# Kernel tuning notes

Hardware: AMD Instinct MI355X
Metric: run time of the kernel (lower is better)

## Reference

```python
import jax, jax.numpy as jnp
import numpy as np

B, T, DIM = 1, 1024, 1024
H = 8
QLR, KVLR = 768, 512
DNOPE, DROPE, DV = 128, 64, 128
DK = DNOPE + DROPE  # 192
EPS = 1e-5


def _rms(x, w):
    return x * jax.lax.rsqrt(jnp.mean(x * x, axis=-1, keepdims=True) + EPS) * w


def _l2norm(x):
    return x * jax.lax.rsqrt(jnp.sum(x * x, axis=-1, keepdims=True) + 1e-6)


def setup_inputs() -> dict:
    key = jax.random.key(0)
    ks = jax.random.split(key, 12)
    std = 0.02
    rnd = lambda k, shape: (jax.random.normal(k, shape, dtype=jnp.float32) * std)
    return {
        'x': jax.random.normal(ks[0], (B, T, DIM), dtype=jnp.float32),
        'cos': jax.random.normal(ks[1], (T, DROPE), dtype=jnp.float32),
        'sin': jax.random.normal(ks[2], (T, DROPE), dtype=jnp.float32),
        'wq_a': rnd(ks[3], (DIM, QLR)),
        'q_norm_w': jnp.ones((QLR,), dtype=jnp.float32),
        'wq_b': rnd(ks[4], (QLR, H * DK)),
        'wkv_a': rnd(ks[5], (DIM, KVLR + DROPE)),
        'kv_norm_w': jnp.ones((KVLR,), dtype=jnp.float32),
        'wkv_b': rnd(ks[6], (KVLR, H * (DNOPE + DV))),
        'wg_w': rnd(ks[7], (DIM, H * DK)),
        'wg_b': jnp.zeros((H * DK,), dtype=jnp.float32),
        'wb': rnd(ks[8], (DIM, H)),
        'wo': rnd(ks[9], (H * DV, DIM)),
    }


def _kda(q, k, v, g, beta):
    # q,k: [B,T,H,DK]; v: [B,T,H,DV]; g: [B,T,H,DK] (log-decay); beta: [B,T,H]
    q = _l2norm(q) * (DK ** -0.5)
    k = _l2norm(k)
    # time-major for scan
    qs = jnp.moveaxis(q, 1, 0)
    ks_ = jnp.moveaxis(k, 1, 0)
    vs = jnp.moveaxis(v, 1, 0)
    gs = jnp.moveaxis(g, 1, 0)
    bs = jnp.moveaxis(beta, 1, 0)

    def step(S, inp):
        q_t, k_t, v_t, g_t, b_t = inp  # [B,H,DK],[B,H,DK],[B,H,DV],[B,H,DK],[B,H]
        S = S * jnp.exp(g_t)[..., None]                       # per-key-dim decay
        u_t = b_t[..., None] * (v_t - jnp.einsum('bhk,bhkv->bhv', k_t, S))
        S = S + k_t[..., None] * u_t[..., None, :]            # rank-1 delta update
        o_t = jnp.einsum('bhk,bhkv->bhv', q_t, S)
        return S, o_t

    S0 = jnp.zeros((B, H, DK, DV), dtype=q.dtype)
    _, o = jax.lax.scan(step, S0, (qs, ks_, vs, gs, bs))
    return jnp.moveaxis(o, 0, 1)  # [B,T,H,DV]


def reference(x, cos, sin, wq_a, q_norm_w, wq_b, wkv_a, kv_norm_w, wkv_b, wg_w, wg_b, wb, wo):
    # cos/sin are accepted but unused, matching the original forward body.
    q = (_rms(x @ wq_a, q_norm_w) @ wq_b).reshape(B, T, H, DK)
    kv_all = x @ wkv_a
    kv_c, k_pe = kv_all[..., :KVLR], kv_all[..., KVLR:]       # [B,T,KVLR],[B,T,DROPE]
    kv = (_rms(kv_c, kv_norm_w) @ wkv_b).reshape(B, T, H, DNOPE + DV)
    k_nope, v = kv[..., :DNOPE], kv[..., DNOPE:]
    k = jnp.concatenate(
        [k_nope, jnp.broadcast_to(k_pe[:, :, None, :], (B, T, H, DROPE))], axis=-1)
    g = jax.nn.log_sigmoid(x @ wg_w + wg_b).reshape(B, T, H, DK)
    beta = jax.nn.sigmoid(x @ wb).reshape(B, T, H)
    o = _kda(q, k, v, g, beta)
    o = jnp.nan_to_num(o, nan=0.0, posinf=10000.0, neginf=-10000.0)
    return o.reshape(B, T, H * DV) @ wo
```

## Files before the change

### kernel.cpp

```cpp
#include <hip/hip_runtime.h>
#include <hip/hip_bf16.h>
#include <math.h>

#define TT 1024
#define DIM 1024
#define HH 8
#define QLR 768
#define KVLR 512
#define DNOPE 128
#define DROPE 64
#define DV 128
#define DK 192
#define HDK (HH*DK)
#define HKV (HH*(DNOPE+DV))

#define OY   0
#define OQ   3072
#define OC   6144
#define OPL  9984
#define OU   10240
#define OLAM 12288
#define PABLK 12480

typedef __attribute__((ext_vector_type(8))) short short8;
typedef __attribute__((ext_vector_type(4))) float f32x4;

__device__ __forceinline__ unsigned short f2bf_rn(float f) {
    unsigned u = __float_as_uint(f);
    unsigned lsb = (u >> 16) & 1u;
    u += 0x7fffu + lsb;
    return (unsigned short)(u >> 16);
}
__device__ __forceinline__ float bf2f(unsigned short h) {
    return __uint_as_float(((unsigned)h) << 16);
}

__global__ __launch_bounds__(256) void wconv(
    const float* __restrict__ W0, unsigned short* __restrict__ H0,
    unsigned short* __restrict__ L0, int K0, int N0, int T0,
    const float* __restrict__ W1, unsigned short* __restrict__ H1,
    unsigned short* __restrict__ L1, int K1, int N1, int T1,
    const float* __restrict__ W2, unsigned short* __restrict__ H2,
    unsigned short* __restrict__ L2, int K2, int N2, int T2)
{
    __shared__ float Ls[64][65];
    int bx = blockIdx.x;
    const float* W; unsigned short* H; unsigned short* L; int K, N;
    if (bx < T0)           { W = W0; H = H0; L = L0; K = K0; N = N0; }
    else if (bx < T0 + T1) { bx -= T0; W = W1; H = H1; L = L1; K = K1; N = N1; }
    else                   { bx -= T0 + T1; W = W2; H = H2; L = L2; K = K2; N = N2; }

    const int NT = N >> 6;
    const int kt = bx / NT, nt = bx - kt * NT;
    const int k0 = kt * 64, n0 = nt * 64;
    const int tid = threadIdx.x;
    const int r = tid >> 2, c = (tid & 3) * 16;

#pragma unroll
    for (int i = 0; i < 4; i++)
        *(float4*)&Ls[r][c + i * 4] =
            *(const float4*)&W[(size_t)(k0 + r) * N + n0 + c + i * 4];
    __syncthreads();

    const int nr = tid >> 2, kc = (tid & 3) * 16;
    unsigned short hb[16], lb[16];
#pragma unroll
    for (int j = 0; j < 16; j++) {
        float v = Ls[kc + j][nr];
        unsigned short h = f2bf_rn(v);
        hb[j] = h;
        lb[j] = f2bf_rn(v - bf2f(h));
    }
    size_t ob = (size_t)(n0 + nr) * K + k0 + kc;
    *(float4*)&H[ob]     = ((float4*)hb)[0];
    *(float4*)&H[ob + 8] = ((float4*)hb)[1];
    *(float4*)&L[ob]     = ((float4*)lb)[0];
    *(float4*)&L[ob + 8] = ((float4*)lb)[1];
}

__global__ __launch_bounds__(256) void aconv(
    const float* __restrict__ A, unsigned short* __restrict__ H,
    unsigned short* __restrict__ L)
{
    int i = (blockIdx.x * 256 + threadIdx.x) * 8;
    float4 v0 = *(const float4*)&A[i];
    float4 v1 = *(const float4*)&A[i + 4];
    float vv[8] = {v0.x, v0.y, v0.z, v0.w, v1.x, v1.y, v1.z, v1.w};
    unsigned short hb[8], lb[8];
#pragma unroll
    for (int j = 0; j < 8; j++) {
        unsigned short h = f2bf_rn(vv[j]);
        hb[j] = h;
        lb[j] = f2bf_rn(vv[j] - bf2f(h));
    }
    *(float4*)&H[i] = *(float4*)hb;
    *(float4*)&L[i] = *(float4*)lb;
}

__global__ __launch_bounds__(256) void gemm_bt(
    const unsigned short* __restrict__ Ah0, const unsigned short* __restrict__ Al0,
    const unsigned short* __restrict__ Bh0, const unsigned short* __restrict__ Bl0,
    float* __restrict__ C0, int K0, int N0, int T0,
    const unsigned short* __restrict__ Ah1, const unsigned short* __restrict__ Al1,
    const unsigned short* __restrict__ Bh1, const unsigned short* __restrict__ Bl1,
    float* __restrict__ C1, int K1, int N1, int T1,
    const unsigned short* __restrict__ Ah2, const unsigned short* __restrict__ Al2,
    const unsigned short* __restrict__ Bh2, const unsigned short* __restrict__ Bl2,
    float* __restrict__ C2, int K2, int N2, int T2)
{
    __shared__ unsigned short Ahs[64 * 40], Als[64 * 40];
    __shared__ unsigned short Bhs[64 * 40], Bls[64 * 40];

    int bx = blockIdx.x;
    const unsigned short *Ah, *Al, *Bh, *Bl; float* C; int K, N;
    if (bx < T0) {
        Ah = Ah0; Al = Al0; Bh = Bh0; Bl = Bl0; C = C0; K = K0; N = N0;
    } else if (bx < T0 + T1) {
        bx -= T0; Ah = Ah1; Al = Al1; Bh = Bh1; Bl = Bl1; C = C1; K = K1; N = N1;
    } else {
        bx -= T0 + T1; Ah = Ah2; Al = Al2; Bh = Bh2; Bl = Bl2; C = C2; K = K2; N = N2;
    }

    const int tid = threadIdx.x;
    const int w = tid >> 6, l = tid & 63;
    const int q = l >> 4, m16 = l & 15;
    const int bm = blockIdx.y * 64, bn = bx * 64;

    const int r0 = tid >> 2, o0 = (tid & 3) * 8;
    const unsigned short* pAh0 = Ah + (size_t)(bm + r0) * K + o0;
    const unsigned short* pAl0 = Al + (size_t)(bm + r0) * K + o0;
    const unsigned short* pBh0 = Bh + (size_t)(bn + r0) * K + o0;
    const unsigned short* pBl0 = Bl + (size_t)(bn + r0) * K + o0;

    f32x4 acc[4];
#pragma unroll
    for (int j = 0; j < 4; j++)
        acc[j] = (f32x4){0.f, 0.f, 0.f, 0.f};

    float4 vAh0 = *(const float4*)pAh0;
    float4 vAl0 = *(const float4*)pAl0;
    float4 vBh0 = *(const float4*)pBh0;
    float4 vBl0 = *(const float4*)pBl0;

    for (int k0 = 0;; k0 += 32) {
        __syncthreads();
        *(float4*)&Ahs[r0 * 40 + o0] = vAh0;
        *(float4*)&Als[r0 * 40 + o0] = vAl0;
        *(float4*)&Bhs[r0 * 40 + o0] = vBh0;
        *(float4*)&Bls[r0 * 40 + o0] = vBl0;
        __syncthreads();

        const bool more = (k0 + 32) < K;
        if (more) {
            const int kn = k0 + 32;
            vAh0 = *(const float4*)(pAh0 + kn);
            vAl0 = *(const float4*)(pAl0 + kn);
            vBh0 = *(const float4*)(pBh0 + kn);
            vBl0 = *(const float4*)(pBl0 + kn);
        }

        short8 fah, fal, fbh[4], fbl[4];
        {
            const int row = w * 16 + m16;
            fah = *(const short8*)&Ahs[row * 40 + q * 8];
            fal = *(const short8*)&Als[row * 40 + q * 8];
        }
#pragma unroll
        for (int nt = 0; nt < 4; nt++) {
            const int row = nt * 16 + m16;
            fbh[nt] = *(const short8*)&Bhs[row * 40 + q * 8];
            fbl[nt] = *(const short8*)&Bls[row * 40 + q * 8];
        }
#pragma unroll
        for (int nt = 0; nt < 4; nt++) {
            acc[nt] = __builtin_amdgcn_mfma_f32_16x16x32_bf16(
                fah, fbh[nt], acc[nt], 0, 0, 0);
            acc[nt] = __builtin_amdgcn_mfma_f32_16x16x32_bf16(
                fah, fbl[nt], acc[nt], 0, 0, 0);
            acc[nt] = __builtin_amdgcn_mfma_f32_16x16x32_bf16(
                fal, fbh[nt], acc[nt], 0, 0, 0);
        }
        if (!more) break;
    }

#pragma unroll
    for (int nt = 0; nt < 4; nt++) {
        const int mrow = bm + w * 16 + q * 4;
        const int ncol = bn + nt * 16 + m16;
#pragma unroll
        for (int r = 0; r < 4; r++)
            C[(size_t)(mrow + r) * N + ncol] = acc[nt][r];
    }
}

__global__ __launch_bounds__(256) void rmsnorm_bf2(
    const float* __restrict__ in0, const float* __restrict__ w0,
    unsigned short* __restrict__ oh0, unsigned short* __restrict__ ol0,
    const float* __restrict__ in1, const float* __restrict__ w1,
    unsigned short* __restrict__ oh1, unsigned short* __restrict__ ol1)
{
    int bx = blockIdx.x;
    const float* in; const float* w; unsigned short *oh, *ol;
    int t, stride, ncols; float inv_n;
    if (bx < TT) {
        t = bx; in = in0; w = w0; oh = oh0; ol = ol0;
        stride = QLR; ncols = QLR; inv_n = 1.f / QLR;
    } else {
        t = bx - TT; in = in1; w = w1; oh = oh1; ol = ol1;
        stride = KVLR + DROPE; ncols = KVLR; inv_n = 1.f / KVLR;
    }
    const int tid = threadIdx.x;
    const float* row = in + (size_t)t * stride;
    float ss = 0.f;
    for (int c = tid; c < ncols; c += 256) { float v = row[c]; ss += v * v; }
#pragma unroll
    for (int m = 1; m < 64; m <<= 1) ss += __shfl_xor(ss, m);
    __shared__ float red[4];
    if ((tid & 63) == 0) red[tid >> 6] = ss;
    __syncthreads();
    float tot = red[0] + red[1] + red[2] + red[3];
    float scale = rsqrtf(tot * inv_n + 1e-5f);
    for (int c = tid; c < ncols; c += 256) {
        float v = row[c] * scale * w[c];
        unsigned short h = f2bf_rn(v);
        oh[(size_t)t * ncols + c] = h;
        ol[(size_t)t * ncols + c] = f2bf_rn(v - bf2f(h));
    }
}

__device__ __forceinline__ float dpp_xor1(float x) {
    return __int_as_float(__builtin_amdgcn_update_dpp(
        0, __float_as_int(x), 0xB1, 0xF, 0xF, false));
}
__device__ __forceinline__ float dpp_xor2(float x) {
    return __int_as_float(__builtin_amdgcn_update_dpp(
        0, __float_as_int(x), 0x4E, 0xF, 0xF, false));
}
__device__ __forceinline__ float dpp_hm(float x) {
    return __int_as_float(__builtin_amdgcn_update_dpp(
        0, __float_as_int(x), 0x141, 0xF, 0xF, false));
}
__device__ __forceinline__ float dpp_rm(float x) {
    return __int_as_float(__builtin_amdgcn_update_dpp(
        0, __float_as_int(x), 0x140, 0xF, 0xF, false));
}
__device__ __forceinline__ float dpp_b15(float x) {
    return __int_as_float(__builtin_amdgcn_update_dpp(
        0, __float_as_int(x), 0x142, 0xF, 0xF, false));
}
__device__ __forceinline__ float red16(float x) {
    x += dpp_xor1(x);
    x += dpp_xor2(x);
    x += dpp_hm(x);
    x += dpp_rm(x);
    return x;
}
__device__ __forceinline__ float red32v(float x) {
    x += dpp_xor1(x);
    x += dpp_xor2(x);
    x += dpp_hm(x);
    x += dpp_rm(x);
    x += dpp_b15(x);
    return x;
}

__device__ __forceinline__ void gl_lds16(const float* g, float* l) {
    __builtin_amdgcn_global_load_lds(
        (const __attribute__((address_space(1))) void*)g,
        (__attribute__((address_space(3))) void*)l, 16, 0, 0);
}

__global__ __launch_bounds__(256) void chunk_prep(
    const float* __restrict__ qnraw, const float* __restrict__ agraw,
    const float* __restrict__ wg_b, const float* __restrict__ kvb,
    const float* __restrict__ kv_all, const float* __restrict__ x,
    const float* __restrict__ wb, float* __restrict__ pa)
{
    __shared__ float Ls[16][196];
    __shared__ float Ks[16][196];
    __shared__ float Qs[16][196];
    __shared__ float Ws[16][196];
    __shared__ float Xs[16][196];
    __shared__ float Ms[16][16];
    __shared__ float bs[16];
    __shared__ float kn[16], qn[16];

    const int tid = threadIdx.x;
    const int n = blockIdx.x >> 3, h = blockIdx.x & 7;
    const int t0 = n * 16;
    float* blob = pa + (size_t)blockIdx.x * PABLK;

#pragma unroll
    for (int s = 0; s < 3; s++) {
        int off = (tid * 3 + s) * 4;
        int r = off / 192, c = off - r * 192;
        *(float4*)&Qs[r][c] =
            *(const float4*)(qnraw + (size_t)(t0 + r) * HDK + h * DK + c);
        float4 g4 = *(const float4*)(agraw + (size_t)(t0 + r) * HDK + h * DK + c);
        float4 b4 = *(const float4*)(wg_b + h * DK + c);
        float4 la;
        {
            float z;
            z = g4.x + b4.x; la.x = fminf(z, 0.f) - log1pf(__expf(-fabsf(z)));
            z = g4.y + b4.y; la.y = fminf(z, 0.f) - log1pf(__expf(-fabsf(z)));
            z = g4.z + b4.z; la.z = fminf(z, 0.f) - log1pf(__expf(-fabsf(z)));
            z = g4.w + b4.w; la.w = fminf(z, 0.f) - log1pf(__expf(-fabsf(z)));
        }
        *(float4*)&Ls[r][c] = la;
        float4 kv;
        if (c < DNOPE)
            kv = *(const float4*)(kvb + (size_t)(t0 + r) * HKV + h * (DNOPE + DV) + c);
        else
            kv = *(const float4*)(kv_all + (size_t)(t0 + r) * (KVLR + DROPE) + KVLR + (c - DNOPE));
        *(float4*)&Ks[r][c] = kv;
    }
    {
        const int lane = tid & 63, wv = tid >> 6;
#pragma unroll
        for (int rr = 0; rr < 4; rr++) {
            const int r = wv * 4 + rr;
            const float* xr = x + (size_t)(t0 + r) * DIM;
            float ssum = 0.f;
            for (int e = lane; e < DIM; e += 64) ssum += xr[e] * wb[e * HH + h];
#pragma unroll
            for (int m = 1; m < 64; m <<= 1) ssum += __shfl_xor(ssum, m);
            if (lane == 0) bs[r] = 1.f / (1.f + expf(-ssum));
        }
    }
    __syncthreads();

    {
        const int i = tid >> 4, j = tid & 15;
        float sq = 0.f, sk = 0.f;
#pragma unroll
        for (int c4 = 0; c4 < 3; c4++) {
            float4 q4 = *(const float4*)&Qs[i][j * 12 + c4 * 4];
            float4 k4 = *(const float4*)&Ks[i][j * 12 + c4 * 4];
            sq += q4.x * q4.x + q4.y * q4.y + q4.z * q4.z + q4.w * q4.w;
            sk += k4.x * k4.x + k4.y * k4.y + k4.z * k4.z + k4.w * k4.w;
        }
        sq = red16(sq);
        sk = red16(sk);
        if (j == 0) {
            qn[i] = rsqrtf(sq + 1e-6f) * 0.07216878364870323f;
            kn[i] = rsqrtf(sk + 1e-6f);
        }
    }
    if (tid < 192) {
        float g = 0.f;
#pragma unroll
        for (int i = 0; i < 16; i++) { g += Ls[i][tid]; Ls[i][tid] = g; }
    }
    __syncthreads();

#pragma unroll
    for (int s = 0; s < 12; s++) {
        int idx = s * 256 + tid;
        int i = idx / 192, d = idx - i * 192;
        float G = Ls[i][d];
        float eg = __expf(G), en = __expf(-G);
        float kk = Ks[i][d] * kn[i];
        Ws[i][d] = bs[i] * kk * eg;
        Qs[i][d] = Qs[i][d] * qn[i] * eg;
        Ks[i][d] = kk * en;
    }
    __syncthreads();

#pragma unroll
    for (int s = 0; s < 3; s++) {
        int off = (tid * 3 + s) * 4;
        int r = off / 192, c = off - r * 192;
        *(float4*)(blob + OQ + off) = *(const float4*)&Qs[r][c];
    }
    if (tid < 192) {
        float lam = __expf(Ls[15][tid]);
        blob[OLAM + tid] = lam;
#pragma unroll
        for (int j4 = 0; j4 < 4; j4++) {
            float4 v;
            v.x = Ks[j4 * 4 + 0][tid] * lam; v.y = Ks[j4 * 4 + 1][tid] * lam;
            v.z = Ks[j4 * 4 + 2][tid] * lam; v.w = Ks[j4 * 4 + 3][tid] * lam;
            *(float4*)(blob + OC + tid * 20 + j4 * 4) = v;
        }
        blob[OC + tid * 20 + 16] = lam;
        blob[OC + tid * 20 + 17] = 0.f;
        blob[OC + tid * 20 + 18] = 0.f; blob[OC + tid * 20 + 19] = 0.f;
    }
    {
        const int i = tid >> 4, j = tid & 15;
        float m = 0.f, p = 0.f;
#pragma unroll
        for (int d4 = 0; d4 < 48; d4++) {
            float4 w  = *(const float4*)&Ws[i][d4 * 4];
            float4 ka = *(const float4*)&Ks[j][d4 * 4];
            float4 qa = *(const float4*)&Qs[i][d4 * 4];
            m += w.x * ka.x + w.y * ka.y + w.z * ka.z + w.w * ka.w;
            p += qa.x * ka.x + qa.y * ka.y + qa.z * ka.z + qa.w * ka.w;
        }
        Ms[i][j] = (j < i) ? m : 0.f;
        blob[OPL + tid] = (j <= i) ? p : 0.f;
    }
    __syncthreads();

    float y[16], uu[16];
    const bool doY = (tid < 192);
    const bool doU = (tid >= 128);
    const int dcol = tid, ccol = tid - 128;
    if (doY) {
#pragma unroll
        for (int i = 0; i < 16; i++) y[i] = Ws[i][dcol];
#pragma unroll
        for (int i = 1; i < 16; i++)
#pragma unroll
            for (int j = 0; j < i; j++)
                y[i] = fmaf(-Ms[i][j], y[j], y[i]);
    }
    if (doU) {
#pragma unroll
        for (int i = 0; i < 16; i++)
            uu[i] = bs[i] * kvb[(size_t)(t0 + i) * HKV + h * (DNOPE + DV) + DNOPE + ccol];
#pragma unroll
        for (int i = 1; i < 16; i++)
#pragma unroll
            for (int j = 0; j < i; j++)
                uu[i] = fmaf(-Ms[i][j], uu[j], uu[i]);
    }
    if (doY) {
#pragma unroll
        for (int i = 0; i < 16; i++) Xs[i][dcol] = y[i];
    }
    __syncthreads();
#pragma unroll
    for (int s = 0; s < 3; s++) {
        int off = (tid * 3 + s) * 4;
        int r = off / 192, c = off - r * 192;
        *(float4*)(blob + OY + off) = *(const float4*)&Xs[r][c];
    }
    if (doU) {
#pragma unroll
        for (int i4 = 0; i4 < 4; i4++) {
            float4 t;
            t.x = uu[i4 * 4 + 0]; t.y = uu[i4 * 4 + 1];
            t.z = uu[i4 * 4 + 2]; t.w = uu[i4 * 4 + 3];
            *(float4*)(blob + OU + (size_t)ccol * 16 + i4 * 4) = t;
        }
    }
}

__global__ __launch_bounds__(1024) void kda_chunk(
    const float* __restrict__ pa, unsigned short* __restrict__ obh,
    unsigned short* __restrict__ obl)
{
    __shared__ float Cb[3][3840];
    __shared__ float Pb[3][256];
    __shared__ float ubs[3][64];
    __shared__ float lbs[3][192];
    __shared__ float Ss[784];
    __shared__ float us[80];

    const int tid = threadIdx.x;
    const int w = tid >> 6, lane = tid & 63;
    const int h = blockIdx.x & 7, cg = blockIdx.x >> 3;
    const int c0 = cg * 4;

    const int ti  = w;
    const int ccs = lane >> 5;
    const int dg  = lane & 31;
    const int dbase = dg * 6;

    auto stage = [&](int buf, int n) {
        const float* blob = pa + (size_t)(n * 8 + h) * PABLK;
        if (w < 15) {
            gl_lds16(blob + OC + w * 256 + lane * 4, &Cb[buf][w * 256]);
        } else {
            gl_lds16(blob + OPL + lane * 4, &Pb[buf][0]);
            if (lane < 16)
                gl_lds16(blob + OU + c0 * 16 + lane * 4, &ubs[buf][0]);
            if (lane < 48)
                gl_lds16(blob + OLAM + lane * 4, &lbs[buf][0]);
        }
    };

    auto ldYQ = [&](int n, float2 (&Y)[3], float2 (&Q)[3]) {
        const float* blob = pa + (size_t)(n * 8 + h) * PABLK;
        const float* py_ = blob + OY + ti * 192 + dbase;
        const float* pq_ = blob + OQ + ti * 192 + dbase;
#pragma unroll
        for (int s = 0; s < 3; s++) {
            Y[s] = *(const float2*)(py_ + s * 2);
            Q[s] = *(const float2*)(pq_ + s * 2);
        }
    };

    auto P1 = [&](int sbase, int bf, float2 (&Yr)[3], float2 (&Qr)[3]) -> float {
        const int r = sbase + ccs;
        const float* Sp = &Ss[r * 196 + dbase];
        float2 s0 = *(const float2*)Sp;
        float2 s1 = *(const float2*)(Sp + 2);
        float2 s2 = *(const float2*)(Sp + 4);
        float ubv = ubs[bf][r * 16 + ti];
        float py0 = Yr[0].x * s0.x, py1 = Yr[0].y * s0.y;
        float pq0 = Qr[0].x * s0.x, pq1 = Qr[0].y * s0.y;
        py0 = fmaf(Yr[1].x, s1.x, py0); py1 = fmaf(Yr[1].y, s1.y, py1);
        pq0 = fmaf(Qr[1].x, s1.x, pq0); pq1 = fmaf(Qr[1].y, s1.y, pq1);
        py0 = fmaf(Yr[2].x, s2.x, py0); py1 = fmaf(Yr[2].y, s2.y, py1);
        pq0 = fmaf(Qr[2].x, s2.x, pq0); pq1 = fmaf(Qr[2].y, s2.y, pq1);
        float zy = red32v(py0 + py1);
        float zq = red32v(pq0 + pq1);
        if (dg == 31) us[r * 20 + ti] = ubv - zy;
        return zq;
    };

    auto P2 = [&](int sbase, int bf, int n, float zq) {
        const int r = sbase + ccs;
        float pbvv = Pb[bf][ti * 16 + (dg & 15)];
        float usv  = us[r * 20 + (dg & 15)];
        float acc = (dg <= ti) ? pbvv * usv : 0.f;
        acc = red32v(acc);
        if (dg == 31) {
            float ov = zq + acc;
            if (isnan(ov)) ov = 0.f;
            else if (isinf(ov)) ov = ov > 0.f ? 1e4f : -1e4f;
            size_t oi = (size_t)(n * 16 + ti) * (HH * DV) + h * DV + c0 + r;
            unsigned short hb = f2bf_rn(ov);
            obh[oi] = hb;
            obl[oi] = f2bf_rn(ov - bf2f(hb));
        }
        if (tid < 384) {
            const int d = tid >> 1, c = (tid & 1) + sbase;
            const float4* up4 = (const float4*)&us[c * 20];
            float4 u0 = up4[0], u1 = up4[1], u2v = up4[2], u3 = up4[3];
            float svv = Ss[c * 196 + d];
            const float4* C4 = (const float4*)&Cb[bf][d * 20];
            float4 k0 = C4[0], k1 = C4[1], k2 = C4[2], k3 = C4[3];
            float a0 = lbs[bf][d] * svv, a1 = 0.f;
            a0 = fmaf(k0.x, u0.x,  a0); a1 = fmaf(k0.y, u0.y,  a1);
            a0 = fmaf(k0.z, u0.z,  a0); a1 = fmaf(k0.w, u0.w,  a1);
            a0 = fmaf(k1.x, u1.x,  a0); a1 = fmaf(k1.y, u1.y,  a1);
            a0 = fmaf(k1.z, u1.z,  a0); a1 = fmaf(k1.w, u1.w,  a1);
            a0 = fmaf(k2.x, u2v.x, a0); a1 = fmaf(k2.y, u2v.y, a1);
            a0 = fmaf(k2.z, u2v.z, a0); a1 = fmaf(k2.w, u2v.w, a1);
            a0 = fmaf(k3.x, u3.x,  a0); a1 = fmaf(k3.y, u3.y,  a1);
            a0 = fmaf(k3.z, u3.z,  a0); a1 = fmaf(k3.w, u3.w,  a1);
            Ss[c * 196 + d] = a0 + a1;
        }
    };

#define SEG_BAR asm volatile("s_waitcnt lgkmcnt(0)\n\ts_barrier" ::: "memory")

    float zqA, zqB;
    float2 Ya[3], Qa[3], Yb[3], Qb[3];

    for (int idx = tid; idx < 784; idx += 1024) Ss[idx] = 0.f;
    stage(0, 0);
    stage(1, 1);
    asm volatile("" ::: "memory");
    ldYQ(0, Ya, Qa);
    asm volatile("s_waitcnt vmcnt(0) lgkmcnt(0)\n\ts_barrier" ::: "memory");
    zqA = P1(0, 0, Ya, Qa);
    SEG_BAR;

    int bf = 0;
    for (int n = 0; n < 62; n += 2) {
        int bf1 = bf + 1; if (bf1 >= 3) bf1 -= 3;
        int bf2 = bf + 2; if (bf2 >= 3) bf2 -= 3;
        stage(bf2, n + 2);
        asm volatile("" ::: "memory");
        ldYQ(n + 1, Yb, Qb);
        zqB = P1(2, bf, Ya, Qa);
        P2(0, bf, n, zqA);
        SEG_BAR;
        zqA = P1(0, bf1, Yb, Qb);
        P2(2, bf, n, zqB);
        SEG_BAR;
        stage(bf, n + 3);
        asm volatile("" ::: "memory");
        ldYQ(n + 2, Ya, Qa);
        zqB = P1(2, bf1, Yb, Qb);
        P2(0, bf1, n + 1, zqA);
        SEG_BAR;
        zqA = P1(0, bf2, Ya, Qa);
        P2(2, bf1, n + 1, zqB);
        SEG_BAR;
        bf = bf2;
    }
    {
        int bf1 = bf + 1; if (bf1 >= 3) bf1 -= 3;
        ldYQ(63, Yb, Qb);
        zqB = P1(2, bf, Ya, Qa);
        P2(0, bf, 62, zqA);
        SEG_BAR;
        zqA = P1(0, bf1, Yb, Qb);
        P2(2, bf, 62, zqB);
        SEG_BAR;
        zqB = P1(2, bf1, Yb, Qb);
        P2(0, bf1, 63, zqA);
        SEG_BAR;
        P2(2, bf1, 63, zqB);
    }
#undef SEG_BAR
}

extern "C" void kernel_launch(void* const* d_in, const int* in_sizes, int n_in,
                              void* d_out, int out_size, void* d_ws, size_t ws_size,
                              hipStream_t stream)
{
    const float* x         = (const float*)d_in[0];
    const float* wq_a      = (const float*)d_in[3];
    const float* q_norm_w  = (const float*)d_in[4];
    const float* wq_b      = (const float*)d_in[5];
    const float* wkv_a     = (const float*)d_in[6];
    const float* kv_norm_w = (const float*)d_in[7];
    const float* wkv_b     = (const float*)d_in[8];
    const float* wg_w      = (const float*)d_in[9];
    const float* wg_b      = (const float*)d_in[10];
    const float* wb        = (const float*)d_in[11];
    const float* wo        = (const float*)d_in[12];
    float* out = (float*)d_out;

    float* ws = (float*)d_ws;
    float* xq     = ws;
    float* kv_all = xq     + TT * QLR;
    float* agraw  = kv_all + TT * (KVLR + DROPE);
    float* qnraw  = agraw  + TT * HDK;
    float* kvb    = qnraw  + TT * HDK;
    float* spare  = kvb    + TT * HKV;
    float* pa     = spare  + 3 * TT * HDK + TT * HH;
    float* tail   = pa     + 512 * PABLK;

    unsigned short* wo_h  = (unsigned short*)tail;
    unsigned short* wo_l  = wo_h  + 1048576;
    unsigned short* xh    = wo_l  + 1048576;
    unsigned short* xl    = xh    + 1048576;
    unsigned short* xqh   = xl    + 1048576;
    unsigned short* xql   = xqh   + 786432;
    unsigned short* kvnh  = xql   + 786432;
    unsigned short* kvnl  = kvnh  + 524288;

    unsigned short* wqa_h  = (unsigned short*)pa;
    unsigned short* wqa_l  = wqa_h  + 786432;
    unsigned short* wkva_h = wqa_l  + 786432;
    unsigned short* wkva_l = wkva_h + 589824;
    unsigned short* wgw_h  = wkva_l + 589824;
    unsigned short* wgw_l  = wgw_h  + 1572864;
    unsigned short* wqb_h  = wgw_l  + 1572864;
    unsigned short* wqb_l  = wqb_h  + 1179648;
    unsigned short* wkvb_h = wqb_l  + 1179648;
    unsigned short* wkvb_l = wkvb_h + 1048576;

    unsigned short* obh = (unsigned short*)spare;
    unsigned short* obl = obh + 1048576;

    dim3 blk(256);

    wconv<<<dim3(192 + 144 + 384), blk, 0, stream>>>(
        wq_a, wqa_h, wqa_l, DIM, QLR, 192,
        wkv_a, wkva_h, wkva_l, DIM, KVLR + DROPE, 144,
        wg_w, wgw_h, wgw_l, DIM, HDK, 384);
    wconv<<<dim3(288 + 256 + 256), blk, 0, stream>>>(
        wq_b, wqb_h, wqb_l, QLR, HDK, 288,
        wkv_b, wkvb_h, wkvb_l, KVLR, HKV, 256,
        wo, wo_h, wo_l, DIM, DIM, 256);

    aconv<<<dim3(TT * DIM / (256 * 8)), blk, 0, stream>>>(x, xh, xl);

    gemm_bt<<<dim3(12 + 9 + 24, 16), dim3(256), 0, stream>>>(
        xh, xl, wqa_h, wqa_l, xq, DIM, QLR, 12,
        xh, xl, wkva_h, wkva_l, kv_all, DIM, KVLR + DROPE, 9,
        xh, xl, wgw_h, wgw_l, agraw, DIM, HDK, 24);

    rmsnorm_bf2<<<dim3(2 * TT), blk, 0, stream>>>(
        xq, q_norm_w, xqh, xql,
        kv_all, kv_norm_w, kvnh, kvnl);

    gemm_bt<<<dim3(24 + 32, 16), dim3(256), 0, stream>>>(
        xqh, xql, wqb_h, wqb_l, qnraw, QLR, HDK, 24,
        kvnh, kvnl, wkvb_h, wkvb_l, kvb, KVLR, HKV, 32,
        xh, xl, wqa_h, wqa_l, xq, DIM, QLR, 0);

    chunk_prep<<<512, blk, 0, stream>>>(
        qnraw, agraw, wg_b, kvb, kv_all, x, wb, pa);
    kda_chunk<<<256, dim3(1024), 0, stream>>>(pa, obh, obl);

    gemm_bt<<<dim3(16, 16), dim3(256), 0, stream>>>(
        obh, obl, wo_h, wo_l, out, DIM, DIM, 16,
        xh, xl, wqa_h, wqa_l, xq, DIM, QLR, 0,
        xh, xl, wqa_h, wqa_l, xq, DIM, QLR, 0);
}
```

Measured before the change: 313.1 us.

## Fold activation conversion into weight-convert kernel and double-buffer GEMM LDS

```diff
diff --git a/kernel.cpp b/kernel.cpp
--- a/kernel.cpp
+++ b/kernel.cpp
@@ -41,10 +41,28 @@
     const float* __restrict__ W1, unsigned short* __restrict__ H1,
     unsigned short* __restrict__ L1, int K1, int N1, int T1,
     const float* __restrict__ W2, unsigned short* __restrict__ H2,
-    unsigned short* __restrict__ L2, int K2, int N2, int T2)
+    unsigned short* __restrict__ L2, int K2, int N2, int T2,
+    const float* __restrict__ A, unsigned short* __restrict__ AH,
+    unsigned short* __restrict__ AL)
 {
     __shared__ float Ls[64][65];
     int bx = blockIdx.x;
+    if (bx >= T0 + T1 + T2) {
+        int i = ((bx - (T0 + T1 + T2)) * 256 + threadIdx.x) * 8;
+        float4 v0 = *(const float4*)&A[i];
+        float4 v1 = *(const float4*)&A[i + 4];
+        float vv[8] = {v0.x, v0.y, v0.z, v0.w, v1.x, v1.y, v1.z, v1.w};
+        unsigned short hb[8], lb[8];
+#pragma unroll
+        for (int j = 0; j < 8; j++) {
+            unsigned short h = f2bf_rn(vv[j]);
+            hb[j] = h;
+            lb[j] = f2bf_rn(vv[j] - bf2f(h));
+        }
+        *(float4*)&AH[i] = *(float4*)hb;
+        *(float4*)&AL[i] = *(float4*)lb;
+        return;
+    }
     const float* W; unsigned short* H; unsigned short* L; int K, N;
     if (bx < T0)           { W = W0; H = H0; L = L0; K = K0; N = N0; }
     else if (bx < T0 + T1) { bx -= T0; W = W1; H = H1; L = L1; K = K1; N = N1; }
@@ -76,25 +94,6 @@
     *(float4*)&H[ob + 8] = ((float4*)hb)[1];
     *(float4*)&L[ob]     = ((float4*)lb)[0];
     *(float4*)&L[ob + 8] = ((float4*)lb)[1];
-}
-
-__global__ __launch_bounds__(256) void aconv(
-    const float* __restrict__ A, unsigned short* __restrict__ H,
-    unsigned short* __restrict__ L)
-{
-    int i = (blockIdx.x * 256 + threadIdx.x) * 8;
-    float4 v0 = *(const float4*)&A[i];
-    float4 v1 = *(const float4*)&A[i + 4];
-    float vv[8] = {v0.x, v0.y, v0.z, v0.w, v1.x, v1.y, v1.z, v1.w};
-    unsigned short hb[8], lb[8];
-#pragma unroll
-    for (int j = 0; j < 8; j++) {
-        unsigned short h = f2bf_rn(vv[j]);
-        hb[j] = h;
-        lb[j] = f2bf_rn(vv[j] - bf2f(h));
-    }
-    *(float4*)&H[i] = *(float4*)hb;
-    *(float4*)&L[i] = *(float4*)lb;
 }
 
 __global__ __launch_bounds__(256) void gemm_bt(
@@ -108,8 +107,8 @@
     const unsigned short* __restrict__ Bh2, const unsigned short* __restrict__ Bl2,
     float* __restrict__ C2, int K2, int N2, int T2)
 {
-    __shared__ unsigned short Ahs[64 * 40], Als[64 * 40];
-    __shared__ unsigned short Bhs[64 * 40], Bls[64 * 40];
+    __shared__ unsigned short Ahs[2][64 * 40], Als[2][64 * 40];
+    __shared__ unsigned short Bhs[2][64 * 40], Bls[2][64 * 40];
 
     int bx = blockIdx.x;
     const unsigned short *Ah, *Al, *Bh, *Bl; float* C; int K, N;
@@ -142,12 +141,12 @@
     float4 vBh0 = *(const float4*)pBh0;
     float4 vBl0 = *(const float4*)pBl0;
 
+    int p = 0;
     for (int k0 = 0;; k0 += 32) {
-        __syncthreads();
-        *(float4*)&Ahs[r0 * 40 + o0] = vAh0;
-        *(float4*)&Als[r0 * 40 + o0] = vAl0;
-        *(float4*)&Bhs[r0 * 40 + o0] = vBh0;
-        *(float4*)&Bls[r0 * 40 + o0] = vBl0;
+        *(float4*)&Ahs[p][r0 * 40 + o0] = vAh0;
+        *(float4*)&Als[p][r0 * 40 + o0] = vAl0;
+        *(float4*)&Bhs[p][r0 * 40 + o0] = vBh0;
+        *(float4*)&Bls[p][r0 * 40 + o0] = vBl0;
         __syncthreads();
 
         const bool more = (k0 + 32) < K;
@@ -162,15 +161,16 @@
         short8 fah, fal, fbh[4], fbl[4];
         {
             const int row = w * 16 + m16;
-            fah = *(const short8*)&Ahs[row * 40 + q * 8];
-            fal = *(const short8*)&Als[row * 40 + q * 8];
+            fah = *(const short8*)&Ahs[p][row * 40 + q * 8];
+            fal = *(const short8*)&Als[p][row * 40 + q * 8];
         }
 #pragma unroll
         for (int nt = 0; nt < 4; nt++) {
             const int row = nt * 16 + m16;
-            fbh[nt] = *(const short8*)&Bhs[row * 40 + q * 8];
-            fbl[nt] = *(const short8*)&Bls[row * 40 + q * 8];
-        }
+            fbh[nt] = *(const short8*)&Bhs[p][row * 40 + q * 8];
+            fbl[nt] = *(const short8*)&Bls[p][row * 40 + q * 8];
+        }
+        __builtin_amdgcn_s_setprio(1);
 #pragma unroll
         for (int nt = 0; nt < 4; nt++) {
             acc[nt] = __builtin_amdgcn_mfma_f32_16x16x32_bf16(
@@ -180,7 +180,9 @@
             acc[nt] = __builtin_amdgcn_mfma_f32_16x16x32_bf16(
                 fal, fbh[nt], acc[nt], 0, 0, 0);
         }
+        __builtin_amdgcn_s_setprio(0);
         if (!more) break;
+        p ^= 1;
     }
 
 #pragma unroll
@@ -653,16 +655,16 @@
 
     dim3 blk(256);
 
-    wconv<<<dim3(192 + 144 + 384), blk, 0, stream>>>(
+    wconv<<<dim3(192 + 144 + 384 + 512), blk, 0, stream>>>(
         wq_a, wqa_h, wqa_l, DIM, QLR, 192,
         wkv_a, wkva_h, wkva_l, DIM, KVLR + DROPE, 144,
-        wg_w, wgw_h, wgw_l, DIM, HDK, 384);
+        wg_w, wgw_h, wgw_l, DIM, HDK, 384,
+        x, xh, xl);
     wconv<<<dim3(288 + 256 + 256), blk, 0, stream>>>(
         wq_b, wqb_h, wqb_l, QLR, HDK, 288,
         wkv_b, wkvb_h, wkvb_l, KVLR, HKV, 256,
-        wo, wo_h, wo_l, DIM, DIM, 256);
-
-    aconv<<<dim3(TT * DIM / (256 * 8)), blk, 0, stream>>>(x, xh, xl);
+        wo, wo_h, wo_l, DIM, DIM, 256,
+        x, xh, xl);
 
     gemm_bt<<<dim3(12 + 9 + 24, 16), dim3(256), 0, stream>>>(
         xh, xl, wqa_h, wqa_l, xq, DIM, QLR, 12,
```

After: 314.3 us. Within noise of the previous version (+0.4%).
